# Kernel optimization log

Hardware: AMD Instinct MI355X
Metric: run time of the kernel (lower is better)

## Reference

```python
import jax, jax.numpy as jnp
import numpy as np

B, N = 1, 384          # batch, N_res
C_Z, C_H, H = 128, 32, 4  # pair channels, per-head hidden, heads
INF = 1.0e9
LN_EPS = 1e-5


def setup_inputs() -> dict:
    key = jax.random.key(0)
    ks = jax.random.split(key, 8)
    s = lambda k, shape: jax.random.normal(k, shape, jnp.float32) * 0.02
    return {
        "z": jax.random.normal(ks[0], (B, N, N, C_Z), jnp.float32),
        "mask": jnp.ones((B, N, N), jnp.float32),
        "ln_gamma": jnp.ones((C_Z,), jnp.float32),
        "ln_beta": jnp.zeros((C_Z,), jnp.float32),
        "w_bias": s(ks[1], (C_Z, H)),          # Linear(c_z, num_heads, bias=False)
        "w_q": s(ks[2], (C_Z, H * C_H)),        # no-bias q/k/v projections
        "w_k": s(ks[3], (C_Z, H * C_H)),
        "w_v": s(ks[4], (C_Z, H * C_H)),
        "w_g": s(ks[5], (C_Z, H * C_H)),        # gating projection
        "b_g": jnp.ones((H * C_H,), jnp.float32),  # gating bias init ones
        "w_o": s(ks[6], (H * C_H, C_Z)),        # output projection
        "b_o": jnp.zeros((C_Z,), jnp.float32),
    }


def reference(z, mask, ln_gamma, ln_beta, w_bias, w_q, w_k, w_v, w_g, b_g, w_o, b_o):
    # ta_type == "starting": no transposes.
    # LayerNorm over c_z
    mu = jnp.mean(z, axis=-1, keepdims=True)
    var = jnp.var(z, axis=-1, keepdims=True)
    zn = (z - mu) * jax.lax.rsqrt(var + LN_EPS) * ln_gamma + ln_beta  # [B,N,N,C_Z]

    # triangle bias: linear(z) -> [B,N,N,H] -> movedim -> [B,H,i,j], broadcast over batch-row axis
    tri_bias = jnp.einsum('bijc,ch->bhij', zn, w_bias)  # [B,H,N,N]
    # mask bias: masked keys get -inf; mask shape [B,i,k] broadcast to [B,i,1,1,k]
    mask_bias = INF * (mask - 1.0)

    wq = w_q.reshape(C_Z, H, C_H)
    wk = w_k.reshape(C_Z, H, C_H)
    wv = w_v.reshape(C_Z, H, C_H)
    q = jnp.einsum('bijc,chd->bijhd', zn, wq) * (C_H ** -0.5)  # scale q
    k = jnp.einsum('bijc,chd->bijhd', zn, wk)
    v = jnp.einsum('bijc,chd->bijhd', zn, wv)

    # attention over the j/k axis per row i: logits [B,i,H,j,k]
    logits = jnp.einsum('bijhd,bikhd->bihjk', q, k)
    logits = logits + mask_bias[:, :, None, None, :] + tri_bias[:, None, :, :, :]
    a = jax.nn.softmax(logits, axis=-1)
    o = jnp.einsum('bihjk,bikhd->bijhd', a, v)  # [B,N,N,H,C_H]

    # gating
    g = jax.nn.sigmoid(jnp.einsum('bijc,ce->bije', zn, w_g) + b_g)  # [B,N,N,H*C_H]
    o = o.reshape(B, N, N, H * C_H) * g
    return jnp.einsum('bije,ec->bijc', o, w_o) + b_o  # [B,N,N,C_Z]
```

## Files before the change

### kernel.cpp

```cpp
#include <hip/hip_runtime.h>

#define NRES 384
#define CZ 128
#define NH 4
#define CH 32
#define NN (NRES * NRES)
#define NNCZ ((size_t)NN * CZ)

typedef unsigned short u16;
typedef __attribute__((ext_vector_type(4))) unsigned short us4;
typedef __attribute__((ext_vector_type(8))) unsigned short us8;
typedef __attribute__((ext_vector_type(8))) short s8;
typedef __attribute__((ext_vector_type(4))) float f4;

__device__ __forceinline__ float bf2f(u16 u) {
  return __uint_as_float(((unsigned)u) << 16);
}
__device__ __forceinline__ u16 f2bf(float f) {
  unsigned u = __float_as_uint(f);
  u += 0x7fffu + ((u >> 16) & 1u);
  return (u16)(u >> 16);
}

template<bool F32>
__device__ __forceinline__ float ld1(const void* p, size_t i) {
  if constexpr (F32) return ((const float*)p)[i];
  else return bf2f(((const u16*)p)[i]);
}

template<bool F32>
__device__ __forceinline__ void ld4v(const void* p, size_t i, float o[4]) {
  if constexpr (F32) {
    const float4 a = *(const float4*)((const float*)p + i);
    o[0] = a.x; o[1] = a.y; o[2] = a.z; o[3] = a.w;
  } else {
    const us4 v = *(const us4*)((const u16*)p + i);
    #pragma unroll
    for (int u = 0; u < 4; ++u) o[u] = bf2f(v[u]);
  }
}

template<bool F32>
__device__ __forceinline__ void ld8(const void* p, size_t i, float o[8]) {
  if constexpr (F32) {
    const float4 a = *(const float4*)((const float*)p + i);
    const float4 b = *(const float4*)((const float*)p + i + 4);
    o[0] = a.x; o[1] = a.y; o[2] = a.z; o[3] = a.w;
    o[4] = b.x; o[5] = b.y; o[6] = b.z; o[7] = b.w;
  } else {
    const us8 v = *(const us8*)((const u16*)p + i);
    #pragma unroll
    for (int u = 0; u < 8; ++u) o[u] = bf2f(v[u]);
  }
}

__global__ void k_probe(const u16* __restrict__ z, int* __restrict__ flag) {
  int weird = 0;
  for (int i = threadIdx.x; i < 256; i += 64) {
    const int e = (z[i] >> 7) & 0xFF;
    if (e < 0x70 || e > 0x8F) weird++;
  }
  #pragma unroll
  for (int m = 1; m < 64; m <<= 1) weird += __shfl_xor(weird, m, 64);
  if (threadIdx.x == 0) *flag = (weird >= 16) ? 1 : 0;
}

template<bool F32>
__global__ __launch_bounds__(256, 2) void k_ln_proj(
    const void* __restrict__ z, const void* __restrict__ gma, const void* __restrict__ bta,
    const void* __restrict__ wbias, const void* __restrict__ wq, const void* __restrict__ wk,
    const void* __restrict__ wv, const void* __restrict__ wg, const void* __restrict__ bg,
    u16* __restrict__ qb, u16* __restrict__ kb, u16* __restrict__ vb, u16* __restrict__ gb,
    float* __restrict__ triT, const int* __restrict__ flag)
{
  if ((*flag != 0) != F32) return;
  __shared__ __align__(16) u16 znl[128 * 136];
  __shared__ __align__(16) u16 WT[CZ * CZ];
  const int t = threadIdx.x;
  const int lane = t & 63;
  const int wid = t >> 6;
  const int n16 = lane & 15;
  const int quad = lane >> 4;
  const int rowBase = blockIdx.x * 128;

  const int c0 = n16 * 8;
  float g8[8], b8[8];
  ld8<F32>(gma, c0, g8);
  ld8<F32>(bta, c0, b8);
  for (int it = 0; it < 8; ++it) {
    const int rl = wid * 32 + it * 4 + quad;
    float x[8];
    ld8<F32>(z, (size_t)(rowBase + rl) * CZ + c0, x);
    float s = 0.f, q2 = 0.f;
    #pragma unroll
    for (int u = 0; u < 8; ++u) { s += x[u]; q2 += x[u] * x[u]; }
    #pragma unroll
    for (int m = 1; m < 16; m <<= 1) {
      s  += __shfl_xor(s, m, 64);
      q2 += __shfl_xor(q2, m, 64);
    }
    const float mu = s * (1.0f / CZ);
    const float rs = rsqrtf(q2 * (1.0f / CZ) - mu * mu + 1e-5f);
    us8 o;
    #pragma unroll
    for (int u = 0; u < 8; ++u) o[u] = f2bf((x[u] - mu) * rs * g8[u] + b8[u]);
    *(us8*)&znl[rl * 136 + c0] = o;
  }
  __syncthreads();

  float wb4[8][4];
  #pragma unroll
  for (int cc = 0; cc < 8; ++cc) ld4v<F32>(wbias, (size_t)(c0 + cc) * NH, wb4[cc]);
  for (int it = 0; it < 8; ++it) {
    const int rl = wid * 32 + it * 4 + quad;
    const us8 zv8 = *(const us8*)&znl[rl * 136 + c0];
    float a0 = 0.f, a1 = 0.f, a2 = 0.f, a3 = 0.f;
    #pragma unroll
    for (int cc = 0; cc < 8; ++cc) {
      const float zv = bf2f(zv8[cc]);
      a0 += zv * wb4[cc][0]; a1 += zv * wb4[cc][1];
      a2 += zv * wb4[cc][2]; a3 += zv * wb4[cc][3];
    }
    #pragma unroll
    for (int m = 1; m < 16; m <<= 1) {
      a0 += __shfl_xor(a0, m, 64); a1 += __shfl_xor(a1, m, 64);
      a2 += __shfl_xor(a2, m, 64); a3 += __shfl_xor(a3, m, 64);
    }
    if (n16 < 4) {
      const float v = (n16 == 0) ? a0 : (n16 == 1) ? a1 : (n16 == 2) ? a2 : a3;
      const int P = rowBase + rl;
      const int aI = P / NRES, bI = P % NRES;
      triT[(size_t)n16 * NN + (size_t)bI * NRES + aI] = v;
    }
  }

  const u16 scl_q = 1;
  for (int arr = 0; arr < 4; ++arr) {
    const void* W = (arr == 0) ? wq : (arr == 1) ? wk : (arr == 2) ? wv : wg;
    __syncthreads();
    #pragma unroll
    for (int it = 0; it < 16; ++it) {
      const int c = (t >> 5) + it * 8;
      const int m0 = (t & 31) * 4;
      float w4[4];
      ld4v<F32>(W, (size_t)c * CZ + m0, w4);
      const int ks = c >> 5, qq = (c >> 3) & 3, j = c & 7;
      #pragma unroll
      for (int mm = 0; mm < 4; ++mm) {
        const int m = m0 + mm;
        WT[ks * 4096 + (((m >> 4) * 4 + qq) * 16 + (m & 15)) * 8 + j] = f2bf(w4[mm]);
      }
    }
    __syncthreads();

    f4 acc[2][8];
    #pragma unroll
    for (int i = 0; i < 2; ++i)
      #pragma unroll
      for (int nt = 0; nt < 8; ++nt) acc[i][nt] = f4{0.f, 0.f, 0.f, 0.f};

    #pragma unroll
    for (int ks = 0; ks < 4; ++ks) {
      s8 a[2], b[8];
      #pragma unroll
      for (int i = 0; i < 2; ++i)
        a[i] = *(const s8*)&WT[ks * 4096 + (((wid * 2 + i) * 4 + quad) * 16 + n16) * 8];
      #pragma unroll
      for (int nt = 0; nt < 8; ++nt)
        b[nt] = *(const s8*)&znl[(nt * 16 + n16) * 136 + ks * 32 + quad * 8];
      #pragma unroll
      for (int i = 0; i < 2; ++i)
        #pragma unroll
        for (int nt = 0; nt < 8; ++nt)
          acc[i][nt] = __builtin_amdgcn_mfma_f32_16x16x32_bf16(a[i], b[nt], acc[i][nt], 0, 0, 0);
    }

    u16* dstb = (arr == 0) ? qb : (arr == 1) ? kb : (arr == 2) ? vb : gb;
    #pragma unroll
    for (int i = 0; i < 2; ++i) {
      const int mt = wid * 2 + i;
      const int och0 = mt * 16 + quad * 4;
      float e4[4];
      if (arr == 3) ld4v<F32>(bg, och0, e4);
      #pragma unroll
      for (int nt = 0; nt < 8; ++nt) {
        us4 o;
        #pragma unroll
        for (int r = 0; r < 4; ++r) {
          float v = acc[i][nt][r];
          if (arr == 0) v *= 0.17677669529663687f;
          else if (arr == 3) v = 1.0f / (1.0f + __expf(-(v + e4[r])));
          o[r] = f2bf(v);
        }
        *(us4*)&dstb[(size_t)(rowBase + nt * 16 + n16) * CZ + och0] = o;
      }
    }
  }
  (void)scl_q;
}

template<bool F32>
__global__ __launch_bounds__(256, 3) void k_attn(
    const u16* __restrict__ qb, const u16* __restrict__ kb, const u16* __restrict__ vb,
    const u16* __restrict__ gb, const float* __restrict__ triT, const void* __restrict__ msk,
    u16* __restrict__ ogb, const int* __restrict__ flag)
{
  if ((*flag != 0) != F32) return;
  __shared__ __align__(16) u16 VB[12 * 4 * 32 * 8];
  __shared__ __align__(16) u16 Pch[4][2][16 * 40];
  __shared__ __align__(16) float mbL[NRES];
  const int t = threadIdx.x;
  const int i = blockIdx.x >> 2;
  const int h = blockIdx.x & 3;
  const size_t base_i = (size_t)i * NRES;

  #pragma unroll
  for (int it = 0; it < 12; ++it) {
    const int idx = t + it * 256;
    const int kk = idx >> 3;
    const int d0 = (idx & 7) * 4;
    const us4 vv = *(const us4*)&vb[(base_i + kk) * CZ + h * CH + d0];
    const int cc2 = kk >> 5;
    const int kap = kk & 31;
    const int p = 2 * (kap & 15) + (kap >> 4);
    u16* vdst = &VB[((cc2 * 4 + (p >> 3)) * 32 + d0) * 8 + (p & 7)];
    vdst[0] = vv[0]; vdst[8] = vv[1]; vdst[16] = vv[2]; vdst[24] = vv[3];
  }
  for (int idx = t; idx < NRES; idx += 256)
    mbL[idx] = 1.0e9f * (ld1<F32>(msk, base_i + idx) - 1.0f);
  __syncthreads();

  const int wid = t >> 6;
  const int lane = t & 63;
  const int n = lane & 15;
  const int quad = lane >> 4;
  const float* trih = triT + (size_t)h * NN;
  u16* pbA = &Pch[wid][0][0];
  u16* pbB = &Pch[wid][1][0];

  for (int pr = wid; pr < 12; pr += 4) {
    const int jrowA = pr * 32;
    const int jrowB = jrowA + 16;
    const s8 aqA = *(const s8*)&qb[(base_i + jrowA + n) * CZ + h * CH + quad * 8];
    const s8 aqB = *(const s8*)&qb[(base_i + jrowB + n) * CZ + h * CH + quad * 8];

    f4 O0A = {0.f,0.f,0.f,0.f}, O1A = {0.f,0.f,0.f,0.f};
    f4 O0B = {0.f,0.f,0.f,0.f}, O1B = {0.f,0.f,0.f,0.f};
    f4 lA = {0.f,0.f,0.f,0.f}, lB = {0.f,0.f,0.f,0.f};
    f4 mA = {-1.0e30f,-1.0e30f,-1.0e30f,-1.0e30f};
    f4 mB = {-1.0e30f,-1.0e30f,-1.0e30f,-1.0e30f};

    s8 bk[4];
    #pragma unroll
    for (int u = 0; u < 4; ++u)
      bk[u] = *(const s8*)&kb[(base_i + u * 16 + n) * CZ + h * CH + quad * 8];

    #pragma unroll 1
    for (int cc = 0; cc < 6; ++cc) {
      f4 SA[4], SB[4];
      #pragma unroll
      for (int u = 0; u < 4; ++u) {
        const f4 z4 = {0.f, 0.f, 0.f, 0.f};
        SA[u] = __builtin_amdgcn_mfma_f32_16x16x32_bf16(aqA, bk[u], z4, 0, 0, 0);
        SB[u] = __builtin_amdgcn_mfma_f32_16x16x32_bf16(aqB, bk[u], z4, 0, 0, 0);
      }
      if (cc < 5) {
        #pragma unroll
        for (int u = 0; u < 4; ++u)
          bk[u] = *(const s8*)&kb[(base_i + ((cc + 1) * 4 + u) * 16 + n) * CZ + h * CH + quad * 8];
      }
      #pragma unroll
      for (int u = 0; u < 4; ++u) {
        const int tt = cc * 4 + u;
        const float mbv = mbL[tt * 16 + n];
        const size_t trow = (size_t)(tt * 16 + n) * NRES;
        const float4 tA = *(const float4*)&trih[trow + jrowA + quad * 4];
        const float4 tB = *(const float4*)&trih[trow + jrowB + quad * 4];
        SA[u][0] += tA.x + mbv; SA[u][1] += tA.y + mbv;
        SA[u][2] += tA.z + mbv; SA[u][3] += tA.w + mbv;
        SB[u][0] += tB.x + mbv; SB[u][1] += tB.y + mbv;
        SB[u][2] += tB.z + mbv; SB[u][3] += tB.w + mbv;
      }
      f4 mxA = SA[0], mxB = SB[0];
      #pragma unroll
      for (int u = 1; u < 4; ++u) {
        #pragma unroll
        for (int r = 0; r < 4; ++r) {
          mxA[r] = fmaxf(mxA[r], SA[u][r]);
          mxB[r] = fmaxf(mxB[r], SB[u][r]);
        }
      }
      #pragma unroll
      for (int sft = 1; sft < 16; sft <<= 1) {
        #pragma unroll
        for (int r = 0; r < 4; ++r) {
          mxA[r] = fmaxf(mxA[r], __shfl_xor(mxA[r], sft, 64));
          mxB[r] = fmaxf(mxB[r], __shfl_xor(mxB[r], sft, 64));
        }
      }
      #pragma unroll
      for (int r = 0; r < 4; ++r) {
        const float mnA = fmaxf(mA[r], mxA[r]);
        const float scA = __expf(mA[r] - mnA);
        mA[r] = mnA;
        O0A[r] *= scA; O1A[r] *= scA; lA[r] *= scA;
        const float mnB = fmaxf(mB[r], mxB[r]);
        const float scB = __expf(mB[r] - mnB);
        mB[r] = mnB;
        O0B[r] *= scB; O1B[r] *= scB; lB[r] *= scB;
      }
      #pragma unroll
      for (int u = 0; u < 4; ++u) {
        #pragma unroll
        for (int r = 0; r < 4; ++r) {
          SA[u][r] = __expf(SA[u][r] - mA[r]);
          lA[r] += SA[u][r];
          SB[u][r] = __expf(SB[u][r] - mB[r]);
          lB[r] += SB[u][r];
        }
      }
      #pragma unroll
      for (int s = 0; s < 2; ++s) {
        #pragma unroll
        for (int r = 0; r < 4; ++r) {
          const unsigned wA = (unsigned)f2bf(SA[2 * s][r]) |
                              ((unsigned)f2bf(SA[2 * s + 1][r]) << 16);
          *(unsigned*)&pbA[(quad * 4 + r) * 40 + n * 2] = wA;
          const unsigned wB = (unsigned)f2bf(SB[2 * s][r]) |
                              ((unsigned)f2bf(SB[2 * s + 1][r]) << 16);
          *(unsigned*)&pbB[(quad * 4 + r) * 40 + n * 2] = wB;
        }
        const int C = cc * 2 + s;
        const s8 apA = *(const s8*)&pbA[n * 40 + quad * 8];
        const s8 apB = *(const s8*)&pbB[n * 40 + quad * 8];
        const s8 bv0 = *(const s8*)&VB[((C * 4 + quad) * 32 + n) * 8];
        const s8 bv1 = *(const s8*)&VB[((C * 4 + quad) * 32 + 16 + n) * 8];
        O0A = __builtin_amdgcn_mfma_f32_16x16x32_bf16(apA, bv0, O0A, 0, 0, 0);
        O1A = __builtin_amdgcn_mfma_f32_16x16x32_bf16(apA, bv1, O1A, 0, 0, 0);
        O0B = __builtin_amdgcn_mfma_f32_16x16x32_bf16(apB, bv0, O0B, 0, 0, 0);
        O1B = __builtin_amdgcn_mfma_f32_16x16x32_bf16(apB, bv1, O1B, 0, 0, 0);
      }
    }

    f4 sA = lA, sB = lB;
    #pragma unroll
    for (int sft = 1; sft < 16; sft <<= 1) {
      #pragma unroll
      for (int r = 0; r < 4; ++r) {
        sA[r] += __shfl_xor(sA[r], sft, 64);
        sB[r] += __shfl_xor(sB[r], sft, 64);
      }
    }
    #pragma unroll
    for (int r = 0; r < 4; ++r) {
      const float ivA = 1.0f / sA[r];
      const size_t rowA = (base_i + jrowA + quad * 4 + r) * CZ + h * CH;
      const float gA0 = bf2f(gb[rowA + n]);
      const float gA1 = bf2f(gb[rowA + 16 + n]);
      ogb[rowA + n]      = f2bf(O0A[r] * ivA * gA0);
      ogb[rowA + 16 + n] = f2bf(O1A[r] * ivA * gA1);
      const float ivB = 1.0f / sB[r];
      const size_t rowB = (base_i + jrowB + quad * 4 + r) * CZ + h * CH;
      const float gB0 = bf2f(gb[rowB + n]);
      const float gB1 = bf2f(gb[rowB + 16 + n]);
      ogb[rowB + n]      = f2bf(O0B[r] * ivB * gB0);
      ogb[rowB + 16 + n] = f2bf(O1B[r] * ivB * gB1);
    }
  }
}

template<bool F32>
__global__ __launch_bounds__(256, 2) void k_out(
    const u16* __restrict__ og, const void* __restrict__ wo, const void* __restrict__ bo,
    void* __restrict__ outp, const int* __restrict__ flag)
{
  if ((*flag != 0) != F32) return;
  __shared__ __align__(16) u16 ol[128 * 136];
  __shared__ __align__(16) u16 WT[CZ * CZ];
  const int t = threadIdx.x;
  const int lane = t & 63;
  const int wid = t >> 6;
  const int n16 = lane & 15;
  const int quad = lane >> 4;
  const int rowBase = blockIdx.x * 128;

  #pragma unroll
  for (int it = 0; it < 8; ++it) {
    const int idx8 = t + it * 256;
    const int r = idx8 >> 4;
    const int c0 = (idx8 & 15) * 8;
    *(us8*)&ol[r * 136 + c0] = *(const us8*)&og[(size_t)(rowBase + r) * CZ + c0];
  }
  #pragma unroll
  for (int it = 0; it < 16; ++it) {
    const int c = (t >> 5) + it * 8;
    const int m0 = (t & 31) * 4;
    float w4[4];
    ld4v<F32>(wo, (size_t)c * CZ + m0, w4);
    const int ks = c >> 5, qq = (c >> 3) & 3, j = c & 7;
    #pragma unroll
    for (int mm = 0; mm < 4; ++mm) {
      const int m = m0 + mm;
      WT[ks * 4096 + (((m >> 4) * 4 + qq) * 16 + (m & 15)) * 8 + j] = f2bf(w4[mm]);
    }
  }
  __syncthreads();

  f4 acc[2][8];
  #pragma unroll
  for (int i = 0; i < 2; ++i)
    #pragma unroll
    for (int nt = 0; nt < 8; ++nt) acc[i][nt] = f4{0.f, 0.f, 0.f, 0.f};

  #pragma unroll
  for (int ks = 0; ks < 4; ++ks) {
    s8 a[2], b[8];
    #pragma unroll
    for (int i = 0; i < 2; ++i)
      a[i] = *(const s8*)&WT[ks * 4096 + (((wid * 2 + i) * 4 + quad) * 16 + n16) * 8];
    #pragma unroll
    for (int nt = 0; nt < 8; ++nt)
      b[nt] = *(const s8*)&ol[(nt * 16 + n16) * 136 + ks * 32 + quad * 8];
    #pragma unroll
    for (int i = 0; i < 2; ++i)
      #pragma unroll
      for (int nt = 0; nt < 8; ++nt)
        acc[i][nt] = __builtin_amdgcn_mfma_f32_16x16x32_bf16(a[i], b[nt], acc[i][nt], 0, 0, 0);
  }

  #pragma unroll
  for (int i = 0; i < 2; ++i) {
    const int och0 = (wid * 2 + i) * 16 + quad * 4;
    float b4[4];
    ld4v<F32>(bo, och0, b4);
    #pragma unroll
    for (int nt = 0; nt < 8; ++nt) {
      const size_t off = (size_t)(rowBase + nt * 16 + n16) * CZ + och0;
      if constexpr (F32) {
        float4 o;
        o.x = acc[i][nt][0] + b4[0]; o.y = acc[i][nt][1] + b4[1];
        o.z = acc[i][nt][2] + b4[2]; o.w = acc[i][nt][3] + b4[3];
        *(float4*)&((float*)outp)[off] = o;
      } else {
        us4 o;
        #pragma unroll
        for (int r = 0; r < 4; ++r) o[r] = f2bf(acc[i][nt][r] + b4[r]);
        *(us4*)&((u16*)outp)[off] = o;
      }
    }
  }
}

extern "C" void kernel_launch(void* const* d_in, const int* in_sizes, int n_in,
                              void* d_out, int out_size, void* d_ws, size_t ws_size,
                              hipStream_t stream) {
  const void* z     = d_in[0];
  const void* msk   = d_in[1];
  const void* gma   = d_in[2];
  const void* bta   = d_in[3];
  const void* wbias = d_in[4];
  const void* wq    = d_in[5];
  const void* wk    = d_in[6];
  const void* wv    = d_in[7];
  const void* wg    = d_in[8];
  const void* bg    = d_in[9];
  const void* wo    = d_in[10];
  const void* bo    = d_in[11];

  char* ws = (char*)d_ws;
  int* flag = (int*)ws;
  u16* qb = (u16*)(ws + 256);
  u16* kb = qb + NNCZ;
  u16* vb = kb + NNCZ;
  u16* gb = vb + NNCZ;
  float* triT = (float*)(gb + NNCZ);
  u16* ogb = qb;

  k_probe<<<dim3(1), dim3(64), 0, stream>>>((const u16*)z, flag);

  k_ln_proj<false><<<dim3(NN / 128), dim3(256), 0, stream>>>(
      z, gma, bta, wbias, wq, wk, wv, wg, bg, qb, kb, vb, gb, triT, flag);
  k_ln_proj<true><<<dim3(NN / 128), dim3(256), 0, stream>>>(
      z, gma, bta, wbias, wq, wk, wv, wg, bg, qb, kb, vb, gb, triT, flag);

  k_attn<false><<<dim3(NRES * NH), dim3(256), 0, stream>>>(
      qb, kb, vb, gb, triT, msk, ogb, flag);
  k_attn<true><<<dim3(NRES * NH), dim3(256), 0, stream>>>(
      qb, kb, vb, gb, triT, msk, ogb, flag);

  k_out<false><<<dim3(NN / 128), dim3(256), 0, stream>>>(ogb, wo, bo, d_out, flag);
  k_out<true><<<dim3(NN / 128), dim3(256), 0, stream>>>(ogb, wo, bo, d_out, flag);
}
```

Measured before the change: 500.1 us.

## Cut attention softmax overhead: exp2 with folded max, hardware bf16 pack, mask skip

The attention kernel now uses exp2 with the log2e scale folded into a negated running max via fma. It packs bf16 pairs with the hardware v_cvt_pk_bf16_f32 instruction instead of software rounding, and skips the mask-bias add when a block detects no masked keys. It also halves the per-wave P staging buffer by reusing one LDS tile for both row halves. Finally it raises launch bounds to 5 blocks per SM and reorders blocks so the head index is the slow dimension. The aim is fewer VALU ops per element and higher occupancy, at the cost of extra serialization between the two half-tile MFMAs and register pressure under the tighter bound.

```diff
diff --git a/kernel.cpp b/kernel.cpp
--- a/kernel.cpp
+++ b/kernel.cpp
@@ -13,6 +13,8 @@
 typedef __attribute__((ext_vector_type(8))) short s8;
 typedef __attribute__((ext_vector_type(4))) float f4;
 
+#define L2E 1.4426950408889634f
+
 __device__ __forceinline__ float bf2f(u16 u) {
   return __uint_as_float(((unsigned)u) << 16);
 }
@@ -20,6 +22,11 @@
   unsigned u = __float_as_uint(f);
   u += 0x7fffu + ((u >> 16) & 1u);
   return (u16)(u >> 16);
+}
+__device__ __forceinline__ unsigned cvtpk(float lo, float hi) {
+  unsigned w;
+  asm("v_cvt_pk_bf16_f32 %0, %1, %2" : "=v"(w) : "v"(lo), "v"(hi));
+  return w;
 }
 
 template<bool F32>
@@ -200,19 +207,23 @@
 }
 
 template<bool F32>
-__global__ __launch_bounds__(256, 3) void k_attn(
+__global__ __launch_bounds__(256, 5) void k_attn(
     const u16* __restrict__ qb, const u16* __restrict__ kb, const u16* __restrict__ vb,
     const u16* __restrict__ gb, const float* __restrict__ triT, const void* __restrict__ msk,
     u16* __restrict__ ogb, const int* __restrict__ flag)
 {
   if ((*flag != 0) != F32) return;
   __shared__ __align__(16) u16 VB[12 * 4 * 32 * 8];
-  __shared__ __align__(16) u16 Pch[4][2][16 * 40];
+  __shared__ __align__(16) u16 Pch[4][16 * 40];
   __shared__ __align__(16) float mbL[NRES];
+  __shared__ int anyM;
   const int t = threadIdx.x;
-  const int i = blockIdx.x >> 2;
-  const int h = blockIdx.x & 3;
+  const int i = blockIdx.x % NRES;
+  const int h = blockIdx.x / NRES;
   const size_t base_i = (size_t)i * NRES;
+
+  if (t == 0) anyM = 0;
+  __syncthreads();
 
   #pragma unroll
   for (int it = 0; it < 12; ++it) {
@@ -226,17 +237,24 @@
     u16* vdst = &VB[((cc2 * 4 + (p >> 3)) * 32 + d0) * 8 + (p & 7)];
     vdst[0] = vv[0]; vdst[8] = vv[1]; vdst[16] = vv[2]; vdst[24] = vv[3];
   }
-  for (int idx = t; idx < NRES; idx += 256)
-    mbL[idx] = 1.0e9f * (ld1<F32>(msk, base_i + idx) - 1.0f);
+  {
+    int loc = 0;
+    for (int idx = t; idx < NRES; idx += 256) {
+      const float mb = 1.0e9f * (ld1<F32>(msk, base_i + idx) - 1.0f);
+      mbL[idx] = mb;
+      if (mb != 0.0f) loc = 1;
+    }
+    if (loc) atomicOr(&anyM, 1);
+  }
   __syncthreads();
+  const bool masked = (anyM != 0);
 
   const int wid = t >> 6;
   const int lane = t & 63;
   const int n = lane & 15;
   const int quad = lane >> 4;
   const float* trih = triT + (size_t)h * NN;
-  u16* pbA = &Pch[wid][0][0];
-  u16* pbB = &Pch[wid][1][0];
+  u16* pb = &Pch[wid][0];
 
   for (int pr = wid; pr < 12; pr += 4) {
     const int jrowA = pr * 32;
@@ -247,8 +265,10 @@
     f4 O0A = {0.f,0.f,0.f,0.f}, O1A = {0.f,0.f,0.f,0.f};
     f4 O0B = {0.f,0.f,0.f,0.f}, O1B = {0.f,0.f,0.f,0.f};
     f4 lA = {0.f,0.f,0.f,0.f}, lB = {0.f,0.f,0.f,0.f};
-    f4 mA = {-1.0e30f,-1.0e30f,-1.0e30f,-1.0e30f};
-    f4 mB = {-1.0e30f,-1.0e30f,-1.0e30f,-1.0e30f};
+    f4 nmA = {-1.0e30f,-1.0e30f,-1.0e30f,-1.0e30f};
+    f4 nmB = {-1.0e30f,-1.0e30f,-1.0e30f,-1.0e30f};
+    nmA = f4{3.0e38f, 3.0e38f, 3.0e38f, 3.0e38f};
+    nmB = f4{3.0e38f, 3.0e38f, 3.0e38f, 3.0e38f};
 
     s8 bk[4];
     #pragma unroll
@@ -272,23 +292,25 @@
       #pragma unroll
       for (int u = 0; u < 4; ++u) {
         const int tt = cc * 4 + u;
-        const float mbv = mbL[tt * 16 + n];
         const size_t trow = (size_t)(tt * 16 + n) * NRES;
         const float4 tA = *(const float4*)&trih[trow + jrowA + quad * 4];
         const float4 tB = *(const float4*)&trih[trow + jrowB + quad * 4];
-        SA[u][0] += tA.x + mbv; SA[u][1] += tA.y + mbv;
-        SA[u][2] += tA.z + mbv; SA[u][3] += tA.w + mbv;
-        SB[u][0] += tB.x + mbv; SB[u][1] += tB.y + mbv;
-        SB[u][2] += tB.z + mbv; SB[u][3] += tB.w + mbv;
-      }
-      f4 mxA = SA[0], mxB = SB[0];
-      #pragma unroll
-      for (int u = 1; u < 4; ++u) {
-        #pragma unroll
-        for (int r = 0; r < 4; ++r) {
-          mxA[r] = fmaxf(mxA[r], SA[u][r]);
-          mxB[r] = fmaxf(mxB[r], SB[u][r]);
+        SA[u][0] += tA.x; SA[u][1] += tA.y; SA[u][2] += tA.z; SA[u][3] += tA.w;
+        SB[u][0] += tB.x; SB[u][1] += tB.y; SB[u][2] += tB.z; SB[u][3] += tB.w;
+      }
+      if (masked) {
+        #pragma unroll
+        for (int u = 0; u < 4; ++u) {
+          const float mbv = mbL[(cc * 4 + u) * 16 + n];
+          #pragma unroll
+          for (int r = 0; r < 4; ++r) { SA[u][r] += mbv; SB[u][r] += mbv; }
         }
+      }
+      f4 mxA, mxB;
+      #pragma unroll
+      for (int r = 0; r < 4; ++r) {
+        mxA[r] = fmaxf(fmaxf(SA[0][r], SA[1][r]), fmaxf(SA[2][r], SA[3][r]));
+        mxB[r] = fmaxf(fmaxf(SB[0][r], SB[1][r]), fmaxf(SB[2][r], SB[3][r]));
       }
       #pragma unroll
       for (int sft = 1; sft < 16; sft <<= 1) {
@@ -300,43 +322,40 @@
       }
       #pragma unroll
       for (int r = 0; r < 4; ++r) {
-        const float mnA = fmaxf(mA[r], mxA[r]);
-        const float scA = __expf(mA[r] - mnA);
-        mA[r] = mnA;
+        const float nmAn = fminf(nmA[r], mxA[r] * (-L2E));
+        const float scA = __builtin_exp2f(nmAn - nmA[r]);
+        nmA[r] = nmAn;
         O0A[r] *= scA; O1A[r] *= scA; lA[r] *= scA;
-        const float mnB = fmaxf(mB[r], mxB[r]);
-        const float scB = __expf(mB[r] - mnB);
-        mB[r] = mnB;
+        const float nmBn = fminf(nmB[r], mxB[r] * (-L2E));
+        const float scB = __builtin_exp2f(nmBn - nmB[r]);
+        nmB[r] = nmBn;
         O0B[r] *= scB; O1B[r] *= scB; lB[r] *= scB;
       }
       #pragma unroll
       for (int u = 0; u < 4; ++u) {
         #pragma unroll
         for (int r = 0; r < 4; ++r) {
-          SA[u][r] = __expf(SA[u][r] - mA[r]);
+          SA[u][r] = __builtin_exp2f(__builtin_fmaf(SA[u][r], L2E, nmA[r]));
           lA[r] += SA[u][r];
-          SB[u][r] = __expf(SB[u][r] - mB[r]);
+          SB[u][r] = __builtin_exp2f(__builtin_fmaf(SB[u][r], L2E, nmB[r]));
           lB[r] += SB[u][r];
         }
       }
       #pragma unroll
       for (int s = 0; s < 2; ++s) {
-        #pragma unroll
-        for (int r = 0; r < 4; ++r) {
-          const unsigned wA = (unsigned)f2bf(SA[2 * s][r]) |
-                              ((unsigned)f2bf(SA[2 * s + 1][r]) << 16);
-          *(unsigned*)&pbA[(quad * 4 + r) * 40 + n * 2] = wA;
-          const unsigned wB = (unsigned)f2bf(SB[2 * s][r]) |
-                              ((unsigned)f2bf(SB[2 * s + 1][r]) << 16);
-          *(unsigned*)&pbB[(quad * 4 + r) * 40 + n * 2] = wB;
-        }
         const int C = cc * 2 + s;
-        const s8 apA = *(const s8*)&pbA[n * 40 + quad * 8];
-        const s8 apB = *(const s8*)&pbB[n * 40 + quad * 8];
         const s8 bv0 = *(const s8*)&VB[((C * 4 + quad) * 32 + n) * 8];
         const s8 bv1 = *(const s8*)&VB[((C * 4 + quad) * 32 + 16 + n) * 8];
+        #pragma unroll
+        for (int r = 0; r < 4; ++r)
+          *(unsigned*)&pb[(quad * 4 + r) * 40 + n * 2] = cvtpk(SA[2 * s][r], SA[2 * s + 1][r]);
+        const s8 apA = *(const s8*)&pb[n * 40 + quad * 8];
         O0A = __builtin_amdgcn_mfma_f32_16x16x32_bf16(apA, bv0, O0A, 0, 0, 0);
         O1A = __builtin_amdgcn_mfma_f32_16x16x32_bf16(apA, bv1, O1A, 0, 0, 0);
+        #pragma unroll
+        for (int r = 0; r < 4; ++r)
+          *(unsigned*)&pb[(quad * 4 + r) * 40 + n * 2] = cvtpk(SB[2 * s][r], SB[2 * s + 1][r]);
+        const s8 apB = *(const s8*)&pb[n * 40 + quad * 8];
         O0B = __builtin_amdgcn_mfma_f32_16x16x32_bf16(apB, bv0, O0B, 0, 0, 0);
         O1B = __builtin_amdgcn_mfma_f32_16x16x32_bf16(apB, bv1, O1B, 0, 0, 0);
       }
```

Measured after the change: 818.9 us. +63.7%, slower.
